# Performance work log

Measured on AMD Instinct MI355X. Metric: run time of the kernel, lower is better.

## Reference

```python
import jax, jax.numpy as jnp
import numpy as np

N_NODES = 50000
N_EDGES = 800000
D = 128


def setup_inputs() -> dict:
    key = jax.random.key(0)
    ks = jax.random.split(key, 5)
    x = jax.random.normal(ks[0], (N_NODES, D), dtype=jnp.float32)
    edge_index = jax.random.randint(ks[1], (2, N_EDGES), 0, N_NODES, dtype=jnp.int64)
    # GCNConv linear weight + bias, and the two DGCN parameters
    Wc = jax.random.normal(ks[2], (D, D), dtype=jnp.float32) / np.sqrt(D)
    bc = jnp.zeros((D,), dtype=jnp.float32)
    W0 = jax.random.normal(ks[3], (D, D), dtype=jnp.float32)
    Wt = jax.random.normal(ks[4], (D, D), dtype=jnp.float32)
    return {"x": x, "edge_index": edge_index, "Wc": Wc, "bc": bc, "W0": W0, "Wt": Wt}


def gcn_conv(x, edge_index, Wc, bc):
    # PyG GCNConv: add self-loops, symmetric normalization D^-1/2 (A+I) D^-1/2,
    # applied to x @ Wc, plus bias.
    n = x.shape[0]
    loops = jnp.arange(n, dtype=edge_index.dtype)
    src = jnp.concatenate([edge_index[0], loops])  # [E+N]
    dst = jnp.concatenate([edge_index[1], loops])
    ones = jnp.ones(src.shape[0], dtype=x.dtype)
    deg = jax.ops.segment_sum(ones, dst, num_segments=n)  # in-degree incl. self-loop
    dinv = jnp.where(deg > 0, jax.lax.rsqrt(deg), 0.0)
    norm = dinv[src] * dinv[dst]  # [E+N]
    xw = x @ Wc  # [N, D]
    msgs = xw[src] * norm[:, None]  # gather + scale  [E+N, D]
    agg = jax.ops.segment_sum(msgs, dst, num_segments=n)  # scatter-add  [N, D]
    return agg + bc


def reference(x, edge_index, Wc, bc, W0, Wt):
    h_neigh = gcn_conv(x, edge_index, Wc, bc)
    h_self = x @ W0
    h_change = (h_neigh - x) @ Wt
    return h_neigh + h_self + h_change
```

## Files before the change

kernel.cpp:

```cpp
#include <hip/hip_runtime.h>

#define N_NODES 50000
#define N_EDGES 800000
#define D 128
#define NB 196
#define CAPB 8192
#define P1_BLOCKS 256
#define EPB ((N_EDGES + P1_BLOCKS - 1) / P1_BLOCKS)
#define CAP 64

typedef __attribute__((ext_vector_type(8))) short short8;
typedef __attribute__((ext_vector_type(4))) float f32x4;

__device__ __forceinline__ unsigned short f2bf(float f) {
    unsigned int u = __builtin_bit_cast(unsigned int, f);
    u += 0x7FFFu + ((u >> 16) & 1u);
    return (unsigned short)(u >> 16);
}
__device__ __forceinline__ float bf2f(unsigned short h) {
    unsigned int u = ((unsigned int)h) << 16;
    return __builtin_bit_cast(float, u);
}

__global__ void k_init(int* __restrict__ gcur) {
    const int t = threadIdx.x;
    if (t < NB) gcur[t] = t * CAPB;
}

__global__ __launch_bounds__(256) void k_part1(const int* __restrict__ src,
                                               const int* __restrict__ dst,
                                               int* __restrict__ gcur,
                                               unsigned int* __restrict__ pbuf) {
    __shared__ unsigned int stage[NB][CAP + 1];
    __shared__ int scnt[NB];
    const int t = threadIdx.x;
    for (int i = t; i < NB; i += 256) scnt[i] = 0;
    __syncthreads();

    const long e0 = (long)blockIdx.x * EPB;
    const long e1 = (e0 + EPB < N_EDGES) ? e0 + EPB : N_EDGES;
    for (long e = e0 + t; e < e1; e += 256) {
        const int s = src[e];
        const int d = dst[e];
        const int b = d >> 8;
        const unsigned int p = ((unsigned int)(d & 255) << 16) | (unsigned int)s;
        const int slot = atomicAdd(&scnt[b], 1);
        if (slot < CAP) {
            stage[b][slot] = p;
        } else {
            const int pos = atomicAdd(&gcur[b], 1);
            pbuf[pos] = p;
        }
    }
    __syncthreads();
    if (t < NB) {
        const int n = (scnt[t] < CAP) ? scnt[t] : CAP;
        if (n > 0) {
            const int pos = atomicAdd(&gcur[t], n);
            for (int i = 0; i < n; ++i) pbuf[pos + i] = stage[t][i];
        }
    }
}

__global__ __launch_bounds__(256) void k_part2(const unsigned int* __restrict__ pbuf,
                                               const int* __restrict__ gcur,
                                               int* __restrict__ row_start,
                                               int* __restrict__ cnt,
                                               float* __restrict__ dinv,
                                               int* __restrict__ esrc) {
    __shared__ int lcnt[256];
    __shared__ int lcur[256];
    __shared__ int stmp[256];
    const int b = blockIdx.x;
    const int t = threadIdx.x;
    const int base = b * CAPB;
    const int n = gcur[b] - base;

    lcnt[t] = 0;
    __syncthreads();
    for (int i = t; i < n; i += 256) atomicAdd(&lcnt[pbuf[base + i] >> 16], 1);
    __syncthreads();

    const int c = lcnt[t];
    stmp[t] = c;
    __syncthreads();
    for (int off = 1; off < 256; off <<= 1) {
        int u = (t >= off) ? stmp[t - off] : 0;
        __syncthreads();
        stmp[t] += u;
        __syncthreads();
    }
    const int ls = base + stmp[t] - c;
    lcur[t] = ls;
    const int node = b * 256 + t;
    if (node < N_NODES) {
        row_start[node] = ls;
        cnt[node] = c;
        dinv[node] = rsqrtf((float)c + 1.0f);
    }
    __syncthreads();

    for (int i = t; i < n; i += 256) {
        const unsigned int p = pbuf[base + i];
        const int pos = atomicAdd(&lcur[p >> 16], 1);
        esrc[pos] = (int)(p & 0xFFFFu);
    }
}

__global__ __launch_bounds__(256) void k_wx(const float* __restrict__ Wc,
                                            const float* __restrict__ W0,
                                            const float* __restrict__ Wt,
                                            const float* __restrict__ bc,
                                            const float* __restrict__ x,
                                            const float* __restrict__ dinv,
                                            unsigned short* __restrict__ Wp,
                                            float* __restrict__ bv,
                                            unsigned short* __restrict__ xd,
                                            unsigned short* __restrict__ gx) {
    __shared__ float sWt[D * D];
    const int t = threadIdx.x;

    if (blockIdx.x < 17) {
        for (int i = t * 4; i < D * D; i += 256 * 4)
            *(float4*)(sWt + i) = *(const float4*)(Wt + i);
        __syncthreads();

        if (blockIdx.x == 16) {
            if (t < D) {
                float acc = bc[t];
#pragma unroll 16
                for (int k = 0; k < D; ++k) acc += bc[k] * sWt[k * D + t];
                bv[t] = acc;
            }
            return;
        }
        const int id = blockIdx.x * 256 + t;
        const int lane = id & 63;
        const int tile = (id >> 6) & 7;
        const int step = id >> 9;
        const int n = tile * 16 + (lane & 15);
        const int kbase = step * 32 + (lane >> 4) * 8;
        unsigned short v[8];
#pragma unroll
        for (int j = 0; j < 8; ++j) {
            const int k = kbase + j;
            float f;
            if (k < D) {
                f = Wc[k * D + n];
#pragma unroll 16
                for (int m = 0; m < D; ++m) f += Wc[k * D + m] * sWt[m * D + n];
            } else {
                f = W0[(k - D) * D + n] - sWt[(k - D) * D + n];
            }
            v[j] = f2bf(f);
        }
        *(uint4*)(Wp + (long)id * 8) = *(uint4*)v;
        return;
    }

    const int gid = (blockIdx.x - 17) * 256 + t;
    const int node = gid >> 4;
    const int c = gid & 15;
    const float di = dinv[node];
    const float4 a = ((const float4*)x)[(long)node * 32 + c * 2];
    const float4 b = ((const float4*)x)[(long)node * 32 + c * 2 + 1];
    const float f[8] = {a.x, a.y, a.z, a.w, b.x, b.y, b.z, b.w};
    unsigned short vd[8], vb[8];
#pragma unroll
    for (int j = 0; j < 8; ++j) {
        vd[j] = f2bf(di * f[j]);
        vb[j] = f2bf(f[j]);
    }
    *(uint4*)(xd + (long)node * 128 + c * 8) = *(uint4*)vd;
    *(uint4*)(gx + (long)node * 256 + 128 + c * 8) = *(uint4*)vb;
}

__global__ __launch_bounds__(256) void k_gather(const unsigned short* __restrict__ xd,
                                                const int* __restrict__ row_start,
                                                const int* __restrict__ cnt,
                                                const int* __restrict__ esrc,
                                                const float* __restrict__ dinv,
                                                unsigned short* __restrict__ gx) {
    const int node = blockIdx.x * 4 + (threadIdx.x >> 6);
    const int lane = threadIdx.x & 63;
    const int c = lane & 15;
    const int s = lane >> 4;
    const int begin = row_start[node];
    const int end = begin + cnt[node];

    float acc[8] = {};
    int i = begin + s;
    for (; i + 12 < end; i += 16) {
        const int a0 = esrc[i];
        const int a1 = esrc[i + 4];
        const int a2 = esrc[i + 8];
        const int a3 = esrc[i + 12];
        const short8 v0 = *(const short8*)(xd + (long)a0 * 128 + c * 8);
        const short8 v1 = *(const short8*)(xd + (long)a1 * 128 + c * 8);
        const short8 v2 = *(const short8*)(xd + (long)a2 * 128 + c * 8);
        const short8 v3 = *(const short8*)(xd + (long)a3 * 128 + c * 8);
#pragma unroll
        for (int j = 0; j < 8; ++j)
            acc[j] += (bf2f((unsigned short)v0[j]) + bf2f((unsigned short)v1[j])) +
                      (bf2f((unsigned short)v2[j]) + bf2f((unsigned short)v3[j]));
    }
    for (; i < end; i += 4) {
        const int a0 = esrc[i];
        const short8 v0 = *(const short8*)(xd + (long)a0 * 128 + c * 8);
#pragma unroll
        for (int j = 0; j < 8; ++j) acc[j] += bf2f((unsigned short)v0[j]);
    }

#pragma unroll
    for (int j = 0; j < 8; ++j) {
        acc[j] += __shfl_xor(acc[j], 16);
        acc[j] += __shfl_xor(acc[j], 32);
    }

    if (s == 0) {
        const float di = dinv[node];
        const short8 xs = *(const short8*)(xd + (long)node * 128 + c * 8);
        unsigned short o[8];
#pragma unroll
        for (int j = 0; j < 8; ++j)
            o[j] = f2bf(di * (acc[j] + bf2f((unsigned short)xs[j])));
        *(uint4*)(gx + (long)node * 256 + c * 8) = *(uint4*)o;
    }
}

__global__ __launch_bounds__(256) void k_mm(const unsigned short* __restrict__ gx,
                                            const unsigned short* __restrict__ Wp,
                                            const float* __restrict__ bv,
                                            float* __restrict__ out) {
    const int tid = threadIdx.x;
    const int wave = tid >> 6;
    const int lane = tid & 63;
    const int quad = lane >> 4;
    const int lr = lane & 15;
    const int row0 = blockIdx.x * 64 + wave * 16;

    int ar = row0 + lr;
    if (ar >= N_NODES) ar = N_NODES - 1;
    const unsigned short* aptr = gx + (long)ar * 256 + quad * 8;

    f32x4 acc[8] = {};

#pragma unroll
    for (int s = 0; s < 8; ++s) {
        const short8 a = *(const short8*)(aptr + s * 32);
#pragma unroll
        for (int t = 0; t < 8; ++t) {
            const short8 b = *(const short8*)(Wp + ((long)(s * 8 + t) * 64 + lane) * 8);
            acc[t] = __builtin_amdgcn_mfma_f32_16x16x32_bf16(a, b, acc[t], 0, 0, 0);
        }
    }

#pragma unroll
    for (int t = 0; t < 8; ++t) {
        const int col = t * 16 + lr;
        const float bvv = bv[col];
#pragma unroll
        for (int r = 0; r < 4; ++r) {
            const int row = row0 + quad * 4 + r;
            if (row < N_NODES) out[(long)row * D + col] = acc[t][r] + bvv;
        }
    }
}

extern "C" void kernel_launch(void* const* d_in, const int* in_sizes, int n_in,
                              void* d_out, int out_size, void* d_ws, size_t ws_size,
                              hipStream_t stream) {
    const float* x  = (const float*)d_in[0];
    const int*   ei = (const int*)d_in[1];
    const float* Wc = (const float*)d_in[2];
    const float* bc = (const float*)d_in[3];
    const float* W0 = (const float*)d_in[4];
    const float* Wt = (const float*)d_in[5];
    float* out = (float*)d_out;

    const int* src = ei;
    const int* dst = ei + N_EDGES;

    unsigned short* xd = (unsigned short*)d_ws;
    unsigned short* gx = xd + (size_t)N_NODES * 128;
    int*   cnt        = (int*)(gx + (size_t)N_NODES * 256);
    int*   row_start  = cnt + N_NODES;
    float* dinv       = (float*)(row_start + N_NODES);
    int*   esrc       = (int*)(dinv + N_NODES);
    unsigned int* pbuf = (unsigned int*)(esrc + (size_t)NB * CAPB);
    float* bv         = (float*)(pbuf + (size_t)NB * CAPB);
    unsigned short* Wp = (unsigned short*)(bv + D);
    int*   gcur       = (int*)(Wp + 256 * D);

    k_init<<<1, 256, 0, stream>>>(gcur);
    k_part1<<<P1_BLOCKS, 256, 0, stream>>>(src, dst, gcur, pbuf);
    k_part2<<<NB, 256, 0, stream>>>(pbuf, gcur, row_start, cnt, dinv, esrc);
    k_wx<<<17 + (N_NODES * 16) / 256, 256, 0, stream>>>(Wc, W0, Wt, bc, x, dinv,
                                                        Wp, bv, xd, gx);
    k_gather<<<N_NODES / 4, 256, 0, stream>>>(xd, row_start, cnt, esrc, dinv, gx);
    k_mm<<<(N_NODES + 63) / 64, 256, 0, stream>>>(gx, Wp, bv, out);
}
```

Measured before the change: 179.7 us.

## Fuse edge partition with weight prep and fuse gather with MFMA matmul

```diff
diff --git a/kernel.cpp b/kernel.cpp
--- a/kernel.cpp
+++ b/kernel.cpp
@@ -3,11 +3,14 @@
 #define N_NODES 50000
 #define N_EDGES 800000
 #define D 128
-#define NB 196
-#define CAPB 8192
-#define P1_BLOCKS 256
-#define EPB ((N_EDGES + P1_BLOCKS - 1) / P1_BLOCKS)
-#define CAP 64
+#define NB 391
+#define CAPB 4928
+#define P1B 256
+#define EPB ((N_EDGES + P1B - 1) / P1B)
+#define CAP 28
+#define WPB 16
+#define XC0 (P1B + WPB + 1)
+#define KA_BLOCKS (XC0 + (N_NODES * 16) / 256)
 
 typedef __attribute__((ext_vector_type(8))) short short8;
 typedef __attribute__((ext_vector_type(4))) float f32x4;
@@ -24,117 +27,62 @@
 
 __global__ void k_init(int* __restrict__ gcur) {
     const int t = threadIdx.x;
-    if (t < NB) gcur[t] = t * CAPB;
-}
-
-__global__ __launch_bounds__(256) void k_part1(const int* __restrict__ src,
-                                               const int* __restrict__ dst,
-                                               int* __restrict__ gcur,
-                                               unsigned int* __restrict__ pbuf) {
-    __shared__ unsigned int stage[NB][CAP + 1];
-    __shared__ int scnt[NB];
-    const int t = threadIdx.x;
-    for (int i = t; i < NB; i += 256) scnt[i] = 0;
-    __syncthreads();
-
-    const long e0 = (long)blockIdx.x * EPB;
-    const long e1 = (e0 + EPB < N_EDGES) ? e0 + EPB : N_EDGES;
-    for (long e = e0 + t; e < e1; e += 256) {
-        const int s = src[e];
-        const int d = dst[e];
-        const int b = d >> 8;
-        const unsigned int p = ((unsigned int)(d & 255) << 16) | (unsigned int)s;
-        const int slot = atomicAdd(&scnt[b], 1);
-        if (slot < CAP) {
-            stage[b][slot] = p;
-        } else {
-            const int pos = atomicAdd(&gcur[b], 1);
-            pbuf[pos] = p;
-        }
-    }
-    __syncthreads();
-    if (t < NB) {
-        const int n = (scnt[t] < CAP) ? scnt[t] : CAP;
-        if (n > 0) {
-            const int pos = atomicAdd(&gcur[t], n);
-            for (int i = 0; i < n; ++i) pbuf[pos + i] = stage[t][i];
-        }
-    }
-}
-
-__global__ __launch_bounds__(256) void k_part2(const unsigned int* __restrict__ pbuf,
-                                               const int* __restrict__ gcur,
-                                               int* __restrict__ row_start,
-                                               int* __restrict__ cnt,
-                                               float* __restrict__ dinv,
-                                               int* __restrict__ esrc) {
-    __shared__ int lcnt[256];
-    __shared__ int lcur[256];
-    __shared__ int stmp[256];
-    const int b = blockIdx.x;
-    const int t = threadIdx.x;
-    const int base = b * CAPB;
-    const int n = gcur[b] - base;
-
-    lcnt[t] = 0;
-    __syncthreads();
-    for (int i = t; i < n; i += 256) atomicAdd(&lcnt[pbuf[base + i] >> 16], 1);
-    __syncthreads();
-
-    const int c = lcnt[t];
-    stmp[t] = c;
-    __syncthreads();
-    for (int off = 1; off < 256; off <<= 1) {
-        int u = (t >= off) ? stmp[t - off] : 0;
-        __syncthreads();
-        stmp[t] += u;
-        __syncthreads();
-    }
-    const int ls = base + stmp[t] - c;
-    lcur[t] = ls;
-    const int node = b * 256 + t;
-    if (node < N_NODES) {
-        row_start[node] = ls;
-        cnt[node] = c;
-        dinv[node] = rsqrtf((float)c + 1.0f);
-    }
-    __syncthreads();
-
-    for (int i = t; i < n; i += 256) {
-        const unsigned int p = pbuf[base + i];
-        const int pos = atomicAdd(&lcur[p >> 16], 1);
-        esrc[pos] = (int)(p & 0xFFFFu);
-    }
-}
-
-__global__ __launch_bounds__(256) void k_wx(const float* __restrict__ Wc,
-                                            const float* __restrict__ W0,
-                                            const float* __restrict__ Wt,
-                                            const float* __restrict__ bc,
-                                            const float* __restrict__ x,
-                                            const float* __restrict__ dinv,
-                                            unsigned short* __restrict__ Wp,
-                                            float* __restrict__ bv,
-                                            unsigned short* __restrict__ xd,
-                                            unsigned short* __restrict__ gx) {
+    if (t < NB) gcur[t] = 0;
+}
+
+__global__ __launch_bounds__(256) void k_a(const int* __restrict__ src,
+                                           const int* __restrict__ dst,
+                                           int* __restrict__ gcur,
+                                           unsigned int* __restrict__ pbuf,
+                                           const float* __restrict__ Wc,
+                                           const float* __restrict__ W0,
+                                           const float* __restrict__ Wt,
+                                           const float* __restrict__ bc,
+                                           const float* __restrict__ x,
+                                           unsigned short* __restrict__ Wp,
+                                           float* __restrict__ bv,
+                                           unsigned short* __restrict__ xb) {
     __shared__ float sWt[D * D];
     const int t = threadIdx.x;
-
-    if (blockIdx.x < 17) {
+    const unsigned int bid = blockIdx.x;
+
+    if (bid < P1B) {
+        unsigned int (*stage)[CAP + 1] =
+            reinterpret_cast<unsigned int(*)[CAP + 1]>(sWt);
+        int* scnt = reinterpret_cast<int*>(sWt) + NB * (CAP + 1);
+        for (int i = t; i < NB; i += 256) scnt[i] = 0;
+        __syncthreads();
+
+        const long e0 = (long)bid * EPB;
+        const long e1 = (e0 + EPB < N_EDGES) ? e0 + EPB : N_EDGES;
+        for (long e = e0 + t; e < e1; e += 256) {
+            const int s = src[e];
+            const int d = dst[e];
+            const int b = d >> 7;
+            const unsigned int p = ((unsigned int)(d & 127) << 16) | (unsigned int)s;
+            const int slot = atomicAdd(&scnt[b], 1);
+            if (slot < CAP) {
+                stage[b][slot] = p;
+            } else {
+                pbuf[(long)b * CAPB + atomicAdd(&gcur[b], 1)] = p;
+            }
+        }
+        __syncthreads();
+        for (int bb = t; bb < NB; bb += 256) {
+            const int n = (scnt[bb] < CAP) ? scnt[bb] : CAP;
+            if (n > 0) {
+                const int pos = bb * CAPB + atomicAdd(&gcur[bb], n);
+                for (int i = 0; i < n; ++i) pbuf[pos + i] = stage[bb][i];
+            }
+        }
+        return;
+    }
+
+    if (bid < P1B + WPB) {
         for (int i = t * 4; i < D * D; i += 256 * 4)
             *(float4*)(sWt + i) = *(const float4*)(Wt + i);
         __syncthreads();
-
-        if (blockIdx.x == 16) {
-            if (t < D) {
-                float acc = bc[t];
-#pragma unroll 16
-                for (int k = 0; k < D; ++k) acc += bc[k] * sWt[k * D + t];
-                bv[t] = acc;
-            }
-            return;
-        }
-        const int id = blockIdx.x * 256 + t;
+        const int id = (int)(bid - P1B) * 256 + t;
         const int lane = id & 63;
         const int tile = (id >> 6) & 7;
         const int step = id >> 9;
@@ -158,111 +106,185 @@
         return;
     }
 
-    const int gid = (blockIdx.x - 17) * 256 + t;
+    if (bid == P1B + WPB) {
+        if (t < D) {
+            float acc = bc[t];
+#pragma unroll 16
+            for (int k = 0; k < D; ++k) acc += bc[k] * Wt[k * D + t];
+            bv[t] = acc;
+        }
+        return;
+    }
+
+    const int gid = (int)(bid - XC0) * 256 + t;
     const int node = gid >> 4;
     const int c = gid & 15;
-    const float di = dinv[node];
     const float4 a = ((const float4*)x)[(long)node * 32 + c * 2];
     const float4 b = ((const float4*)x)[(long)node * 32 + c * 2 + 1];
     const float f[8] = {a.x, a.y, a.z, a.w, b.x, b.y, b.z, b.w};
-    unsigned short vd[8], vb[8];
-#pragma unroll
-    for (int j = 0; j < 8; ++j) {
-        vd[j] = f2bf(di * f[j]);
-        vb[j] = f2bf(f[j]);
-    }
-    *(uint4*)(xd + (long)node * 128 + c * 8) = *(uint4*)vd;
-    *(uint4*)(gx + (long)node * 256 + 128 + c * 8) = *(uint4*)vb;
-}
-
-__global__ __launch_bounds__(256) void k_gather(const unsigned short* __restrict__ xd,
-                                                const int* __restrict__ row_start,
-                                                const int* __restrict__ cnt,
-                                                const int* __restrict__ esrc,
-                                                const float* __restrict__ dinv,
-                                                unsigned short* __restrict__ gx) {
-    const int node = blockIdx.x * 4 + (threadIdx.x >> 6);
-    const int lane = threadIdx.x & 63;
-    const int c = lane & 15;
-    const int s = lane >> 4;
-    const int begin = row_start[node];
-    const int end = begin + cnt[node];
-
-    float acc[8] = {};
-    int i = begin + s;
-    for (; i + 12 < end; i += 16) {
-        const int a0 = esrc[i];
-        const int a1 = esrc[i + 4];
-        const int a2 = esrc[i + 8];
-        const int a3 = esrc[i + 12];
-        const short8 v0 = *(const short8*)(xd + (long)a0 * 128 + c * 8);
-        const short8 v1 = *(const short8*)(xd + (long)a1 * 128 + c * 8);
-        const short8 v2 = *(const short8*)(xd + (long)a2 * 128 + c * 8);
-        const short8 v3 = *(const short8*)(xd + (long)a3 * 128 + c * 8);
-#pragma unroll
-        for (int j = 0; j < 8; ++j)
-            acc[j] += (bf2f((unsigned short)v0[j]) + bf2f((unsigned short)v1[j])) +
-                      (bf2f((unsigned short)v2[j]) + bf2f((unsigned short)v3[j]));
-    }
-    for (; i < end; i += 4) {
-        const int a0 = esrc[i];
-        const short8 v0 = *(const short8*)(xd + (long)a0 * 128 + c * 8);
-#pragma unroll
-        for (int j = 0; j < 8; ++j) acc[j] += bf2f((unsigned short)v0[j]);
-    }
-
-#pragma unroll
-    for (int j = 0; j < 8; ++j) {
-        acc[j] += __shfl_xor(acc[j], 16);
-        acc[j] += __shfl_xor(acc[j], 32);
-    }
-
-    if (s == 0) {
-        const float di = dinv[node];
-        const short8 xs = *(const short8*)(xd + (long)node * 128 + c * 8);
-        unsigned short o[8];
-#pragma unroll
-        for (int j = 0; j < 8; ++j)
-            o[j] = f2bf(di * (acc[j] + bf2f((unsigned short)xs[j])));
-        *(uint4*)(gx + (long)node * 256 + c * 8) = *(uint4*)o;
-    }
-}
-
-__global__ __launch_bounds__(256) void k_mm(const unsigned short* __restrict__ gx,
-                                            const unsigned short* __restrict__ Wp,
-                                            const float* __restrict__ bv,
-                                            float* __restrict__ out) {
+    unsigned short vb[8];
+#pragma unroll
+    for (int j = 0; j < 8; ++j) vb[j] = f2bf(f[j]);
+    *(uint4*)(xb + (long)node * 128 + c * 8) = *(uint4*)vb;
+}
+
+__global__ __launch_bounds__(256) void k_part2(const unsigned int* __restrict__ pbuf,
+                                               const int* __restrict__ gcur,
+                                               int* __restrict__ row_start,
+                                               int* __restrict__ cnt,
+                                               float* __restrict__ dinv,
+                                               int* __restrict__ esrc) {
+    __shared__ int lcnt[128];
+    __shared__ int lcur[128];
+    __shared__ int stmp[128];
+    const int b = blockIdx.x;
+    const int t = threadIdx.x;
+    const int base = b * CAPB;
+    const int n = gcur[b];
+
+    if (t < 128) lcnt[t] = 0;
+    __syncthreads();
+    for (int i = t; i < n; i += 256) atomicAdd(&lcnt[pbuf[base + i] >> 16], 1);
+    __syncthreads();
+
+    int c = 0;
+    if (t < 128) {
+        c = lcnt[t];
+        stmp[t] = c;
+    }
+    __syncthreads();
+    for (int off = 1; off < 128; off <<= 1) {
+        int u = (t >= off && t < 128) ? stmp[t - off] : 0;
+        __syncthreads();
+        if (t < 128) stmp[t] += u;
+        __syncthreads();
+    }
+    if (t < 128) {
+        const int ls = base + stmp[t] - c;
+        lcur[t] = ls;
+        const int node = b * 128 + t;
+        if (node < N_NODES) {
+            row_start[node] = ls;
+            cnt[node] = c;
+            dinv[node] = rsqrtf((float)c + 1.0f);
+        }
+    }
+    __syncthreads();
+
+    for (int i = t; i < n; i += 256) {
+        const unsigned int p = pbuf[base + i];
+        const int pos = atomicAdd(&lcur[p >> 16], 1);
+        esrc[pos] = (int)(p & 0xFFFFu);
+    }
+}
+
+__global__ __launch_bounds__(256) void k_gmm(const unsigned short* __restrict__ xb,
+                                             const int* __restrict__ row_start,
+                                             const int* __restrict__ cnt,
+                                             const float* __restrict__ dinv,
+                                             const int* __restrict__ esrc,
+                                             const unsigned short* __restrict__ Wp,
+                                             const float* __restrict__ bv,
+                                             float* __restrict__ out) {
+    __shared__ unsigned short sg[64 * 128];
     const int tid = threadIdx.x;
     const int wave = tid >> 6;
     const int lane = tid & 63;
+    const int c = lane & 15;
+    const int s = lane >> 4;
+    const int row0 = blockIdx.x * 64;
+
+    for (int m = 0; m < 16; ++m) {
+        const int node = row0 + wave * 16 + m;
+        const bool valid = node < N_NODES;
+        float acc[8] = {};
+        if (valid) {
+            const int begin = row_start[node];
+            const int end = begin + cnt[node];
+            int i = begin + s;
+            for (; i + 12 < end; i += 16) {
+                const int a0 = esrc[i];
+                const int a1 = esrc[i + 4];
+                const int a2 = esrc[i + 8];
+                const int a3 = esrc[i + 12];
+                const short8 v0 = *(const short8*)(xb + (long)a0 * 128 + c * 8);
+                const short8 v1 = *(const short8*)(xb + (long)a1 * 128 + c * 8);
+                const short8 v2 = *(const short8*)(xb + (long)a2 * 128 + c * 8);
+                const short8 v3 = *(const short8*)(xb + (long)a3 * 128 + c * 8);
+                const float d0 = dinv[a0];
+                const float d1 = dinv[a1];
+                const float d2 = dinv[a2];
+                const float d3 = dinv[a3];
+#pragma unroll
+                for (int j = 0; j < 8; ++j)
+                    acc[j] += (d0 * bf2f((unsigned short)v0[j]) +
+                               d1 * bf2f((unsigned short)v1[j])) +
+                              (d2 * bf2f((unsigned short)v2[j]) +
+                               d3 * bf2f((unsigned short)v3[j]));
+            }
+            for (; i < end; i += 4) {
+                const int a0 = esrc[i];
+                const float d0 = dinv[a0];
+                const short8 v0 = *(const short8*)(xb + (long)a0 * 128 + c * 8);
+#pragma unroll
+                for (int j = 0; j < 8; ++j) acc[j] += d0 * bf2f((unsigned short)v0[j]);
+            }
+        }
+#pragma unroll
+        for (int j = 0; j < 8; ++j) {
+            acc[j] += __shfl_xor(acc[j], 16);
+            acc[j] += __shfl_xor(acc[j], 32);
+        }
+        if (s == 0) {
+            const int r = wave * 16 + m;
+            unsigned short o[8] = {0, 0, 0, 0, 0, 0, 0, 0};
+            if (valid) {
+                const float di = dinv[node];
+                const short8 xs = *(const short8*)(xb + (long)node * 128 + c * 8);
+#pragma unroll
+                for (int j = 0; j < 8; ++j)
+                    o[j] = f2bf(di * (acc[j] + di * bf2f((unsigned short)xs[j])));
+            }
+            const int col = (c * 16) ^ ((r & 7) << 4);
+            *(uint4*)((char*)sg + r * 256 + col) = *(uint4*)o;
+        }
+    }
+    __syncthreads();
+
+    const int lr = lane & 15;
     const int quad = lane >> 4;
-    const int lr = lane & 15;
-    const int row0 = blockIdx.x * 64 + wave * 16;
-
-    int ar = row0 + lr;
+    const int rloc = wave * 16 + lr;
+    int ar = row0 + rloc;
     if (ar >= N_NODES) ar = N_NODES - 1;
-    const unsigned short* aptr = gx + (long)ar * 256 + quad * 8;
-
-    f32x4 acc[8] = {};
-
-#pragma unroll
-    for (int s = 0; s < 8; ++s) {
-        const short8 a = *(const short8*)(aptr + s * 32);
-#pragma unroll
-        for (int t = 0; t < 8; ++t) {
-            const short8 b = *(const short8*)(Wp + ((long)(s * 8 + t) * 64 + lane) * 8);
-            acc[t] = __builtin_amdgcn_mfma_f32_16x16x32_bf16(a, b, acc[t], 0, 0, 0);
-        }
-    }
-
-#pragma unroll
-    for (int t = 0; t < 8; ++t) {
-        const int col = t * 16 + lr;
+    const unsigned short* aptr = xb + (long)ar * 128 + quad * 8;
+
+    f32x4 acc2[8] = {};
+#pragma unroll
+    for (int s8 = 0; s8 < 8; ++s8) {
+        short8 a;
+        if (s8 < 4) {
+            const int colb = (s8 * 64 + quad * 16) ^ ((rloc & 7) << 4);
+            a = *(const short8*)((const char*)sg + rloc * 256 + colb);
+        } else {
+            a = *(const short8*)(aptr + (s8 - 4) * 32);
+        }
+#pragma unroll
+        for (int t2 = 0; t2 < 8; ++t2) {
+            const short8 b =
+                *(const short8*)(Wp + ((long)(s8 * 8 + t2) * 64 + lane) * 8);
+            acc2[t2] = __builtin_amdgcn_mfma_f32_16x16x32_bf16(a, b, acc2[t2], 0, 0, 0);
+        }
+    }
+
+    const int rowbase = row0 + wave * 16;
+#pragma unroll
+    for (int t2 = 0; t2 < 8; ++t2) {
+        const int col = t2 * 16 + lr;
         const float bvv = bv[col];
 #pragma unroll
         for (int r = 0; r < 4; ++r) {
-            const int row = row0 + quad * 4 + r;
-            if (row < N_NODES) out[(long)row * D + col] = acc[t][r] + bvv;
+            const int row = rowbase + quad * 4 + r;
+            if (row < N_NODES) out[(long)row * D + col] = acc2[t2][r] + bvv;
         }
     }
 }
@@ -281,9 +303,8 @@
     const int* src = ei;
     const int* dst = ei + N_EDGES;
 
-    unsigned short* xd = (unsigned short*)d_ws;
-    unsigned short* gx = xd + (size_t)N_NODES * 128;
-    int*   cnt        = (int*)(gx + (size_t)N_NODES * 256);
+    unsigned short* xb = (unsigned short*)d_ws;
+    int*   cnt        = (int*)(xb + (size_t)N_NODES * 128);
     int*   row_start  = cnt + N_NODES;
     float* dinv       = (float*)(row_start + N_NODES);
     int*   esrc       = (int*)(dinv + N_NODES);
@@ -292,11 +313,10 @@
     unsigned short* Wp = (unsigned short*)(bv + D);
     int*   gcur       = (int*)(Wp + 256 * D);
 
-    k_init<<<1, 256, 0, stream>>>(gcur);
-    k_part1<<<P1_BLOCKS, 256, 0, stream>>>(src, dst, gcur, pbuf);
+    k_init<<<1, 512, 0, stream>>>(gcur);
+    k_a<<<KA_BLOCKS, 256, 0, stream>>>(src, dst, gcur, pbuf, Wc, W0, Wt, bc, x,
+                                       Wp, bv, xb);
     k_part2<<<NB, 256, 0, stream>>>(pbuf, gcur, row_start, cnt, dinv, esrc);
-    k_wx<<<17 + (N_NODES * 16) / 256, 256, 0, stream>>>(Wc, W0, Wt, bc, x, dinv,
-                                                        Wp, bv, xd, gx);
-    k_gather<<<N_NODES / 4, 256, 0, stream>>>(xd, row_start, cnt, esrc, dinv, gx);
-    k_mm<<<(N_NODES + 63) / 64, 256, 0, stream>>>(gx, Wp, bv, out);
-}
+    k_gmm<<<(N_NODES + 63) / 64, 256, 0, stream>>>(xb, row_start, cnt, dinv, esrc,
+                                                   Wp, bv, out);
+}
```

Result: no change. 182.3 us (+1.4%).
